# Optimization experiments

Hardware: AMD Instinct MI355X
Metric: run time of the kernel (lower is better)

The kernel has to match this reference:

```python
import jax, jax.numpy as jnp
import numpy as np

LMAX = 10
F_IN = 64
F_OUT = 64
N_GRID = 512
B = 512


def setup_inputs() -> dict:
    key = jax.random.key(0)
    k1, k2, k3 = jax.random.split(key, 3)
    x = jax.random.normal(k1, (B, F_IN, (LMAX + 1) ** 2), dtype=jnp.float32)
    w = jax.random.normal(k2, (F_IN, F_OUT, N_GRID), dtype=jnp.float32)
    Y = jax.random.normal(k3, (N_GRID, (LMAX + 1) ** 2), dtype=jnp.float32)
    return {"x": x, "w": w, "Y": Y}


def reference(x, w, Y):
    # Project spatial filter into harmonic (fourier) domain.
    # psi: (f_in, f_out, (lmax+1)^2), one scalar weight per (l, u) output mult slot
    n_grid = Y.shape[0]
    psi = jnp.einsum('ni,xyn->xyi', Y, w) / (n_grid ** 0.5)

    lmax = int(round(Y.shape[1] ** 0.5)) - 1
    f_in = w.shape[0]
    f_out = w.shape[1]
    alpha = 1.0 / (f_in ** 0.5)  # e3nn Linear path normalization (mul_in=1)

    outs = []
    for l in range(lmax + 1):  # structural loop over irrep degrees (11 blocks)
        d = 2 * l + 1
        xs = x[:, :, l * l:(l + 1) * (l + 1)]     # (B, f_in, d)  single input copy of irrep l
        ws = psi[:, :, l * l:(l + 1) * (l + 1)]    # (f_in, f_out, d) -> d = output multiplicity u
        # out block: (B, f_out, mult=d, m=d)
        o = jnp.einsum('egu,bem->bgum', ws, xs) * alpha
        outs.append(o.reshape(x.shape[0], f_out, d * d))
    return jnp.concatenate(outs, axis=-1)  # (B, f_out, sum_l (2l+1)^2)
```

## Files before the change

### kernel.cpp

```cpp
#include <hip/hip_runtime.h>
#include <hip/hip_bf16.h>


#define OUTROW 1771
#define OUTB   113344

typedef __attribute__((ext_vector_type(8))) short bf16x8;
typedef __attribute__((ext_vector_type(4))) float floatx4;

__device__ __constant__ int c_off[11] = {0,1,10,35,84,165,286,455,680,969,1330};
__device__ __constant__ signed char c_ltab[121] = {
  0,
  1,1,1,
  2,2,2,2,2,
  3,3,3,3,3,3,3,
  4,4,4,4,4,4,4,4,4,
  5,5,5,5,5,5,5,5,5,5,5,
  6,6,6,6,6,6,6,6,6,6,6,6,6,
  7,7,7,7,7,7,7,7,7,7,7,7,7,7,7,
  8,8,8,8,8,8,8,8,8,8,8,8,8,8,8,8,8,
  9,9,9,9,9,9,9,9,9,9,9,9,9,9,9,9,9,9,9,
  10,10,10,10,10,10,10,10,10,10,10,10,10,10,10,10,10,10,10,10,10
};

__global__ __launch_bounds__(256) void prep_kernel(
    const float* __restrict__ x, const float* __restrict__ w,
    const float* __restrict__ Y,
    __hip_bfloat16* __restrict__ psi_t, __hip_bfloat16* __restrict__ x_t)
{
  __shared__ float smem[8256];
  const int t = threadIdx.x;

  if (blockIdx.x < 512) {
    const int g  = blockIdx.x & 63;
    const int e0 = (blockIdx.x >> 6) * 8;
    float* Ych = smem;
    float* wch = smem + 7744;

    const int i  = t & 127;
    const int es = t >> 7;
    float acc[4] = {0.f, 0.f, 0.f, 0.f};

    for (int n0 = 0; n0 < 512; n0 += 64) {
      __syncthreads();
      {
        const float4* src = (const float4*)(Y + n0*121);
        float4* dst = (float4*)Ych;
        for (int idx = t; idx < 1936; idx += 256) dst[idx] = src[idx];
      }
      {
        int el = t >> 6, k = t & 63;
        wch[el*64 + k]       = w[((e0 + el    )*64 + g)*512 + n0 + k];
        wch[(el+4)*64 + k]   = w[((e0 + el + 4)*64 + g)*512 + n0 + k];
      }
      __syncthreads();
      #pragma unroll 4
      for (int k = 0; k < 64; ++k) {
        float y = Ych[k*121 + i];
        #pragma unroll
        for (int c = 0; c < 4; ++c)
          acc[c] += wch[(es*4 + c)*64 + k] * y;
      }
    }
    if (i < 121) {
      const float scale = 0.00552427172801990267f;
      int l = c_ltab[i];
      int d = 2*l + 1;
      int row = 64*l*l + g*d + (i - l*l);
      __hip_bfloat16* dst = psi_t + row*64 + e0 + es*4;
      ushort4 v;
      __hip_bfloat16 h0 = __float2bfloat16(acc[0]*scale);
      __hip_bfloat16 h1 = __float2bfloat16(acc[1]*scale);
      __hip_bfloat16 h2 = __float2bfloat16(acc[2]*scale);
      __hip_bfloat16 h3 = __float2bfloat16(acc[3]*scale);
      v.x = *(unsigned short*)&h0; v.y = *(unsigned short*)&h1;
      v.z = *(unsigned short*)&h2; v.w = *(unsigned short*)&h3;
      *(ushort4*)dst = v;
    }
  } else {
    const int b = blockIdx.x - 512;
    {
      const float4* src = (const float4*)(x + b*7744);
      float4* dst = (float4*)smem;
      for (int idx = t; idx < 1936; idx += 256) dst[idx] = src[idx];
    }
    __syncthreads();
    const int wv = t >> 6, lane = t & 63;
    for (int ii = wv; ii < 121; ii += 4) {
      int l = c_ltab[ii];
      int d = 2*l + 1;
      int row = 512*l*l + b*d + (ii - l*l);
      x_t[row*64 + lane] = __float2bfloat16(smem[lane*121 + ii]);
    }
  }
}

__global__ __launch_bounds__(256) void conv_kernel(
    const __hip_bfloat16* __restrict__ psi_t,
    const __hip_bfloat16* __restrict__ x_t,
    float* __restrict__ out)
{
  const int bid = blockIdx.x;
  int l = 0;
  #pragma unroll
  for (int ll = 1; ll <= 10; ++ll)
    if (bid >= 2*c_off[ll]) l = ll;
  const int d = 2*l + 1;
  const int r = bid - 2*c_off[l];
  const int qtiles = 2*d;
  const int ptile = r / qtiles;
  const int qtile = r - ptile*qtiles;
  const int p0 = ptile*64, q0 = qtile*256;

  const int t = threadIdx.x;
  const int wv = t >> 6, lane = t & 63;
  const int ln15 = lane & 15, quad = lane >> 4;
  const int pw = p0 + wv*16;

  const ushort* psiRow = (const ushort*)psi_t + (64*l*l + pw + ln15)*64 + quad*8;
  const bf16x8 af0 = *(const bf16x8*)(psiRow);
  const bf16x8 af1 = *(const bf16x8*)(psiRow + 32);

  int rowoff[4];
  #pragma unroll
  for (int rr = 0; rr < 4; ++rr) {
    int p  = pw + quad*4 + rr;
    int gg = p / d;
    int uu = p - gg*d;
    rowoff[rr] = gg*OUTROW + uu*d;
  }
  const int offl = c_off[l];
  const ushort* xbase = (const ushort*)x_t + 512*l*l*64 + quad*8;

  const int stepd = 16 / d;
  const int stepm = 16 - stepd*d;
  int qlane = q0 + ln15;
  int bb = qlane / d;
  int mm = qlane - bb*d;

  #pragma unroll 4
  for (int qq = 0; qq < 16; ++qq) {
    const ushort* xr = xbase + (q0 + qq*16 + ln15)*64;
    bf16x8 bf0 = *(const bf16x8*)(xr);
    bf16x8 bf1 = *(const bf16x8*)(xr + 32);
    floatx4 acc = {0.f, 0.f, 0.f, 0.f};
    acc = __builtin_amdgcn_mfma_f32_16x16x32_bf16(af0, bf0, acc, 0, 0, 0);
    acc = __builtin_amdgcn_mfma_f32_16x16x32_bf16(af1, bf1, acc, 0, 0, 0);
    const int base = bb*OUTB + offl + mm;
    #pragma unroll
    for (int rr = 0; rr < 4; ++rr)
      out[base + rowoff[rr]] = acc[rr];
    bb += stepd; mm += stepm;
    if (mm >= d) { mm -= d; ++bb; }
  }
}

extern "C" void kernel_launch(void* const* d_in, const int* in_sizes, int n_in,
                              void* d_out, int out_size, void* d_ws, size_t ws_size,
                              hipStream_t stream) {
  const float* x = (const float*)d_in[0];
  const float* w = (const float*)d_in[1];
  const float* Y = (const float*)d_in[2];
  float* out = (float*)d_out;

  __hip_bfloat16* psi_t = (__hip_bfloat16*)d_ws;
  __hip_bfloat16* x_t   = (__hip_bfloat16*)((char*)d_ws + (1 << 20));

  prep_kernel<<<1024, 256, 0, stream>>>(x, w, Y, psi_t, x_t);
  conv_kernel<<<3542, 256, 0, stream>>>(psi_t, x_t, out);
}
```

Before: 357.2 us.

## Compute psi projection with split-bf16 MFMA instead of scalar FP32 FMAs

The psi projection (Y^T·w) moves from a scalar FP32 dot loop over 512 blocks to 64 blocks. Each block computes a full output channel with MFMA 16x16x32 bf16, using a hi/lo bf16 split (three MFMAs per tile) to keep near-FP32 accuracy. w is now read straight from global memory as float4 and converted per lane, while Y stays in LDS. This cuts FP32 ALU work in the prep kernel, at the cost of far fewer blocks for that phase, extra conversion work, and strided LDS reads of Y.

```diff
diff --git a/kernel.cpp b/kernel.cpp
--- a/kernel.cpp
+++ b/kernel.cpp
@@ -31,54 +31,91 @@
   __shared__ float smem[8256];
   const int t = threadIdx.x;
 
-  if (blockIdx.x < 512) {
-    const int g  = blockIdx.x & 63;
-    const int e0 = (blockIdx.x >> 6) * 8;
-    float* Ych = smem;
-    float* wch = smem + 7744;
-
-    const int i  = t & 127;
-    const int es = t >> 7;
-    float acc[4] = {0.f, 0.f, 0.f, 0.f};
+  if (blockIdx.x < 64) {
+    const int g    = blockIdx.x;
+    const int wv   = t >> 6, lane = t & 63;
+    const int ln15 = lane & 15, quad = lane >> 4;
+
+    floatx4 acc[2][4] = {};
 
     for (int n0 = 0; n0 < 512; n0 += 64) {
       __syncthreads();
       {
         const float4* src = (const float4*)(Y + n0*121);
-        float4* dst = (float4*)Ych;
+        float4* dst = (float4*)smem;
         for (int idx = t; idx < 1936; idx += 256) dst[idx] = src[idx];
       }
-      {
-        int el = t >> 6, k = t & 63;
-        wch[el*64 + k]       = w[((e0 + el    )*64 + g)*512 + n0 + k];
-        wch[(el+4)*64 + k]   = w[((e0 + el + 4)*64 + g)*512 + n0 + k];
+      __syncthreads();
+
+      #pragma unroll
+      for (int ks = 0; ks < 2; ++ks) {
+        const int kb = ks*32 + quad*8;
+
+        bf16x8 ahi[2], alo[2];
+        #pragma unroll
+        for (int ti = 0; ti < 2; ++ti) {
+          const int irow = (wv << 5) + (ti << 4) + ln15;
+          #pragma unroll
+          for (int j = 0; j < 8; ++j) {
+            float v = smem[(kb + j)*121 + irow];
+            __hip_bfloat16 h = __float2bfloat16(v);
+            float hf = __bfloat162float(h);
+            __hip_bfloat16 lo = __float2bfloat16(v - hf);
+            ahi[ti][j] = *(short*)&h;
+            alo[ti][j] = *(short*)&lo;
+          }
+        }
+
+        bf16x8 bhi[4], blo[4];
+        #pragma unroll
+        for (int te = 0; te < 4; ++te) {
+          const int e = (te << 4) + ln15;
+          const float* wp = w + ((e << 6) + g)*512 + n0 + kb;
+          float4 wa = *(const float4*)wp;
+          float4 wb = *(const float4*)(wp + 4);
+          float v[8] = {wa.x, wa.y, wa.z, wa.w, wb.x, wb.y, wb.z, wb.w};
+          #pragma unroll
+          for (int j = 0; j < 8; ++j) {
+            __hip_bfloat16 h = __float2bfloat16(v[j]);
+            float hf = __bfloat162float(h);
+            __hip_bfloat16 lo = __float2bfloat16(v[j] - hf);
+            bhi[te][j] = *(short*)&h;
+            blo[te][j] = *(short*)&lo;
+          }
+        }
+
+        #pragma unroll
+        for (int ti = 0; ti < 2; ++ti) {
+          #pragma unroll
+          for (int te = 0; te < 4; ++te) {
+            acc[ti][te] = __builtin_amdgcn_mfma_f32_16x16x32_bf16(ahi[ti], bhi[te], acc[ti][te], 0, 0, 0);
+            acc[ti][te] = __builtin_amdgcn_mfma_f32_16x16x32_bf16(ahi[ti], blo[te], acc[ti][te], 0, 0, 0);
+            acc[ti][te] = __builtin_amdgcn_mfma_f32_16x16x32_bf16(alo[ti], bhi[te], acc[ti][te], 0, 0, 0);
+          }
+        }
       }
-      __syncthreads();
-      #pragma unroll 4
-      for (int k = 0; k < 64; ++k) {
-        float y = Ych[k*121 + i];
-        #pragma unroll
-        for (int c = 0; c < 4; ++c)
-          acc[c] += wch[(es*4 + c)*64 + k] * y;
+    }
+
+    const float scale = 0.00552427172801990267f;
+    #pragma unroll
+    for (int ti = 0; ti < 2; ++ti) {
+      #pragma unroll
+      for (int rr = 0; rr < 4; ++rr) {
+        const int i = (wv << 5) + (ti << 4) + (quad << 2) + rr;
+        if (i < 121) {
+          int l = c_ltab[i];
+          int d = 2*l + 1;
+          int row = 64*l*l + g*d + (i - l*l);
+          #pragma unroll
+          for (int te = 0; te < 4; ++te) {
+            __hip_bfloat16 hv = __float2bfloat16(acc[ti][te][rr] * scale);
+            psi_t[row*64 + (te << 4) + ln15] = hv;
+          }
+        }
       }
     }
-    if (i < 121) {
-      const float scale = 0.00552427172801990267f;
-      int l = c_ltab[i];
-      int d = 2*l + 1;
-      int row = 64*l*l + g*d + (i - l*l);
-      __hip_bfloat16* dst = psi_t + row*64 + e0 + es*4;
-      ushort4 v;
-      __hip_bfloat16 h0 = __float2bfloat16(acc[0]*scale);
-      __hip_bfloat16 h1 = __float2bfloat16(acc[1]*scale);
-      __hip_bfloat16 h2 = __float2bfloat16(acc[2]*scale);
-      __hip_bfloat16 h3 = __float2bfloat16(acc[3]*scale);
-      v.x = *(unsigned short*)&h0; v.y = *(unsigned short*)&h1;
-      v.z = *(unsigned short*)&h2; v.w = *(unsigned short*)&h3;
-      *(ushort4*)dst = v;
-    }
   } else {
-    const int b = blockIdx.x - 512;
+    const int b = blockIdx.x - 64;
     {
       const float4* src = (const float4*)(x + b*7744);
       float4* dst = (float4*)smem;
@@ -166,6 +203,6 @@
   __hip_bfloat16* psi_t = (__hip_bfloat16*)d_ws;
   __hip_bfloat16* x_t   = (__hip_bfloat16*)((char*)d_ws + (1 << 20));
 
-  prep_kernel<<<1024, 256, 0, stream>>>(x, w, Y, psi_t, x_t);
+  prep_kernel<<<576, 256, 0, stream>>>(x, w, Y, psi_t, x_t);
   conv_kernel<<<3542, 256, 0, stream>>>(psi_t, x_t, out);
 }
```

New measurement: 355.0 us. No clear change (-0.6%).
